# Optimization experiments

Measured on AMD Instinct MI355X. Metric: run time of the kernel, lower is better.

## Reference

```python
import jax, jax.numpy as jnp
import numpy as np

B, S, DM, H = 4, 1024, 1024, 16
DK = DM // H  # 64, must equal embeddim=64

def _linear(x, W, b):
    # torch nn.Linear: y = x @ W.T + b, W is [out, in]
    return jnp.matmul(x, W.T) + b

def setup_inputs() -> dict:
    key = jax.random.key(0)
    ks = jax.random.split(key, 40)
    inp = {}
    inp["query"] = jax.random.normal(ks[0], (B, S, DM), jnp.float32)
    inp["key"] = jax.random.normal(ks[1], (B, S, DM), jnp.float32)
    inp["value"] = jax.random.normal(ks[2], (B, S, DM), jnp.float32)
    inp["mask"] = jnp.ones((B, S, S), jnp.int32)
    def mk(i, dout, din):
        W = jax.random.normal(ks[i], (dout, din), jnp.float32) / np.sqrt(din).astype(np.float32)
        b = jax.random.normal(ks[i + 20], (dout,), jnp.float32) * 0.01
        return W, b
    # the 4 d_model x d_model projection linears (q, k, v, out)
    inp["Wq"], inp["bq"] = mk(3, DM, DM)
    inp["Wk"], inp["bk"] = mk(4, DM, DM)
    inp["Wv"], inp["bv"] = mk(5, DM, DM)
    inp["Wo"], inp["bo"] = mk(6, DM, DM)
    # the 64x64 refinement linears
    inp["Wkl"], inp["bkl"] = mk(7, DK, DK)   # key_linear
    inp["Wql"], inp["bql"] = mk(8, DK, DK)   # query_linear
    inp["Wq2"], inp["bq2"] = mk(9, DK, DK)   # query2_linear
    inp["Wvl"], inp["bvl"] = mk(10, DK, DK)  # value_linear
    inp["Wel"], inp["bel"] = mk(11, DK, DK)  # embed_linear
    return inp

def reference(query, key, value, mask,
              Wq, bq, Wk, bk, Wv, bv, Wo, bo,
              Wkl, bkl, Wql, bql, Wq2, bq2, Wvl, bvl, Wel, bel):
    b, s, dm = query.shape
    # project and split heads: [b, h, s, d_k]
    def split(x):
        return x.reshape(b, s, H, DK).transpose(0, 2, 1, 3)
    q = split(_linear(query, Wq, bq))
    k = split(_linear(key, Wk, bk))
    v = split(_linear(value, Wv, bv))
    # per-head 64x64 refinements with relu
    key_refine = jax.nn.relu(_linear(k, Wkl, bkl))
    q1 = jax.nn.relu(_linear(q, Wql, bql))
    q1 = jax.nn.relu(_linear(q1, Wel, bel))
    q2 = jax.nn.relu(_linear(q, Wq2, bq2))
    v_refine = jax.nn.relu(_linear(v, Wvl, bvl))
    # two attention-like matmuls (no 1/sqrt(d_k) scaling in original)
    qv = jnp.einsum("bhqd,bhkd->bhqk", q2, v_refine)
    kq = jnp.einsum("bhqd,bhkd->bhqk", q1, key_refine)
    m = mask[:, None, :, :]  # mask.unsqueeze(1)
    kq = jnp.where(m == 0, jnp.float32(-1e9), kq)
    attn = jax.nn.softmax(kq, axis=-1)
    # elementwise combine, then matmul against raw projected key (not value!)
    out = jnp.einsum("bhqk,bhkd->bhqd", attn * qv, k)
    out = out.transpose(0, 2, 1, 3).reshape(b, s, dm)
    return _linear(out, Wo, bo)
```

## Files before the change

kernel.cpp:

```cpp
#include <hip/hip_runtime.h>
#include <hip/hip_bf16.h>

#define B_  4
#define S_  1024
#define DM_ 1024
#define H_  16
#define DK_ 64
#define LOG2E 1.4426950408889634f

typedef unsigned short u16;
typedef __attribute__((ext_vector_type(8))) short bf16x8;
typedef __attribute__((ext_vector_type(4))) float f32x4;

__device__ __forceinline__ float bf2f(u16 u) {
    union { unsigned int i; float f; } c;
    c.i = ((unsigned int)u) << 16;
    return c.f;
}
__device__ __forceinline__ u16 f2bf(float f) {
    union { float f; unsigned int i; } c;
    c.f = f;
    unsigned int x = c.i;
    unsigned int lsb = (x >> 16) & 1u;
    x += 0x7fffu + lsb;
    return (u16)(x >> 16);
}
__device__ __forceinline__ u16 f2bf_fast(float f) {
    __hip_bfloat16 h = __float2bfloat16(f);
    return *reinterpret_cast<u16*>(&h);
}

__device__ __forceinline__ void async_ld16(const u16* g, u16* l) {
    __builtin_amdgcn_global_load_lds(
        (const __attribute__((address_space(1))) unsigned int*)(const void*)g,
        (__attribute__((address_space(3))) unsigned int*)(void*)l, 16, 0, 0);
}

__global__ void detect_kernel(const u16* __restrict__ q, int* __restrict__ flag) {
    int lane = threadIdx.x & 63;
    int cnt = 0;
#pragma unroll
    for (int i = 0; i < 4; ++i) {
        u16 u = q[2 * (lane * 4 + i)];
        int e = (u >> 7) & 0xFF;
        cnt += (e >= 100 && e <= 140) ? 1 : 0;
    }
#pragma unroll
    for (int off = 1; off < 64; off <<= 1) cnt += __shfl_xor(cnt, off, 64);
    if (lane == 0) *flag = (cnt < 128) ? 1 : 0;
}

#define NSEG 12
struct CvtArgs {
    const void* src[NSEG];
    void*       dst[NSEG];
    unsigned    off[NSEG + 1];
};

__global__ __launch_bounds__(256) void prep_kernel(
    CvtArgs a, unsigned total, const int* __restrict__ flag,
    const int* __restrict__ mask, int* __restrict__ tflags)
{
    const int tid = threadIdx.x;
    if (blockIdx.x < 512) {
        const int bx = blockIdx.x;
        const int kt = bx & 15, b = (bx >> 4) & 3, z = bx >> 6;
        int ok = 1;
#pragma unroll
        for (int i = tid; i < 128 * 16; i += 256) {
            int row = z * 128 + (i >> 4), seg = i & 15;
            int4 m = *(const int4*)&mask[((size_t)b * S_ + row) * S_ + kt * 64 + seg * 4];
            ok &= (m.x != 0) & (m.y != 0) & (m.z != 0) & (m.w != 0);
        }
        if (!ok) atomicOr(&tflags[b * 16 + kt], 1);
        return;
    }
    if (!*flag) return;
    unsigned v = (blockIdx.x - 512) * 256 + tid;
    if (v >= total) return;
    int s = 0;
    while (s < NSEG - 1 && v >= a.off[s + 1]) ++s;
    unsigned local = v - a.off[s];
    u16* dp = (u16*)a.dst[s] + (size_t)local * 8;
    const float* sp = (const float*)a.src[s] + (size_t)local * 8;
    float4 x = *(const float4*)sp, y = *(const float4*)(sp + 4);
    u16 t[8] = {f2bf(x.x), f2bf(x.y), f2bf(x.z), f2bf(x.w),
                f2bf(y.x), f2bf(y.y), f2bf(y.z), f2bf(y.w)};
    *(uint4*)dp = *(uint4*)t;
}

__global__ __launch_bounds__(256) void transpose_kernel(
    const u16* __restrict__ kp, u16* __restrict__ kpt)
{
    __shared__ u16 T[64][65];
    const int s0 = blockIdx.x * 64, h = blockIdx.y, b = blockIdx.z;
    const int tid = threadIdx.x;
    const size_t base = (size_t)b * S_ * DM_ + (size_t)h * DK_;
    for (int c = tid; c < 512; c += 256) {
        int row = c >> 3, cc = (c & 7) * 8;
        union { uint4 v; u16 u[8]; } x;
        x.v = *(const uint4*)&kp[base + (size_t)(s0 + row) * DM_ + cc];
#pragma unroll
        for (int j = 0; j < 8; ++j) T[row][cc + j] = x.u[j];
    }
    __syncthreads();
    const size_t baseT = (size_t)(b * H_ + h) * DK_ * S_;
    for (int c = tid; c < 512; c += 256) {
        int d = c >> 3, ss = (c & 7) * 8;
        u16 t[8];
#pragma unroll
        for (int j = 0; j < 8; ++j) t[j] = T[ss + j][d];
        *(uint4*)&kpt[baseT + (size_t)d * S_ + s0 + ss] = *(uint4*)t;
    }
}

struct GemmBatch {
    const u16* A0[4]; const u16* A1[4];
    const u16* W0[4]; const u16* W1[4];
    const u16* W20[4]; const u16* W21[4];
    const void* bias[4];
    const void* bias2[4];
    void* C[4];
    float oscale[4];
    int chain[4];
};

template<int ACT, int BIAS_DYN, int OUT_DYN>
__global__ __launch_bounds__(256, 3) void gemm_async_kernel(
    GemmBatch gb, int M, int N, int K, const int* __restrict__ flag)
{
    __shared__ __align__(16) u16 As[128][64];
    __shared__ __align__(16) u16 Ws[128][64];

    const int g = blockIdx.z;
    const int f = *flag;
    const u16* __restrict__ A = f ? gb.A1[g] : gb.A0[g];
    const u16* __restrict__ W = f ? gb.W1[g] : gb.W0[g];
    const void* biasp = gb.bias[g];
    void* Cp = gb.C[g];

    const int m0   = blockIdx.y * 128;
    const int n0   = blockIdx.x * 128;
    const int tid  = threadIdx.x;
    const int w    = tid >> 6;
    const int lane = tid & 63;
    const int l16  = lane & 15;
    const int quad = lane >> 4;
    const int wr   = (w >> 1) * 64;
    const int wc   = (w & 1) * 64;

    const int srow = lane >> 3;
    const int sgrp = (lane & 7) ^ srow;

    f32x4 acc[4][4];
#pragma unroll
    for (int rt = 0; rt < 4; ++rt)
#pragma unroll
        for (int ct = 0; ct < 4; ++ct) acc[rt][ct] = (f32x4){0.f, 0.f, 0.f, 0.f};

    for (int k0 = 0; k0 < K; k0 += 64) {
#pragma unroll
        for (int s = 0; s < 4; ++s) {
            int seg = w * 4 + s;
            async_ld16(&A[(size_t)(m0 + seg * 8 + srow) * K + k0 + sgrp * 8],
                       &As[seg * 8][0]);
            async_ld16(&W[(size_t)(n0 + seg * 8 + srow) * K + k0 + sgrp * 8],
                       &Ws[seg * 8][0]);
        }
        __syncthreads();
#pragma unroll
        for (int kk = 0; kk < 2; ++kk) {
            const int p = (kk * 4 + quad) ^ (l16 & 7);
            bf16x8 av[4], bv[4];
#pragma unroll
            for (int rt = 0; rt < 4; ++rt)
                av[rt] = *(const bf16x8*)&As[wr + rt * 16 + l16][p * 8];
#pragma unroll
            for (int ct = 0; ct < 4; ++ct)
                bv[ct] = *(const bf16x8*)&Ws[wc + ct * 16 + l16][p * 8];
#pragma unroll
            for (int rt = 0; rt < 4; ++rt)
#pragma unroll
                for (int ct = 0; ct < 4; ++ct)
                    acc[rt][ct] = __builtin_amdgcn_mfma_f32_16x16x32_bf16(
                        av[rt], bv[ct], acc[rt][ct], 0, 0, 0);
        }
        __syncthreads();
    }

#pragma unroll
    for (int ct = 0; ct < 4; ++ct) {
        int col = n0 + wc + ct * 16 + l16;
        float bv = (BIAS_DYN && f) ? ((const float*)biasp)[col]
                                   : bf2f(((const u16*)biasp)[col]);
#pragma unroll
        for (int rt = 0; rt < 4; ++rt)
#pragma unroll
            for (int r = 0; r < 4; ++r) {
                int row = m0 + wr + rt * 16 + quad * 4 + r;
                float v = acc[rt][ct][r] + bv;
                if (ACT) v = v > 0.f ? v : 0.f;
                size_t idx = (size_t)row * N + col;
                if (OUT_DYN && f) ((float*)Cp)[idx] = v;
                else              ((u16*)Cp)[idx]   = f2bf(v);
            }
    }
}

template<int ACT, int BIAS_DYN, int OUT_DYN>
__global__ __launch_bounds__(256, 2) void gemm_small_kernel(
    GemmBatch gb, int M, int N, int K, const int* __restrict__ flag)
{
    __shared__ __align__(16) u16 As[128][72];
    __shared__ __align__(16) u16 Ws[64][72];

    const int g = blockIdx.z;
    const int f = *flag;
    const u16* __restrict__ A = f ? gb.A1[g] : gb.A0[g];
    const u16* __restrict__ W = f ? gb.W1[g] : gb.W0[g];
    const void* biasp = gb.bias[g];
    void* Cp = gb.C[g];
    const float osc = gb.oscale[g];
    const int chain = gb.chain[g];

    const int m0   = blockIdx.y * 128;
    const int n0   = blockIdx.x * 64;
    const int tid  = threadIdx.x;
    const int w    = tid >> 6;
    const int lane = tid & 63;
    const int l16  = lane & 15;
    const int quad = lane >> 4;

    f32x4 acc[2][4];
#pragma unroll
    for (int rt = 0; rt < 2; ++rt)
#pragma unroll
        for (int ct = 0; ct < 4; ++ct) acc[rt][ct] = (f32x4){0.f, 0.f, 0.f, 0.f};

    for (int k0 = 0; k0 < K; k0 += 64) {
#pragma unroll
        for (int c = tid; c < 1024; c += 256) {
            int row = c >> 3, cc = (c & 7) * 8;
            *(uint4*)&As[row][cc] = *(const uint4*)&A[(size_t)(m0 + row) * K + k0 + cc];
        }
#pragma unroll
        for (int c = tid; c < 512; c += 256) {
            int row = c >> 3, cc = (c & 7) * 8;
            *(uint4*)&Ws[row][cc] = *(const uint4*)&W[(size_t)(n0 + row) * K + k0 + cc];
        }
        __syncthreads();
#pragma unroll
        for (int kk = 0; kk < 2; ++kk) {
            bf16x8 a[2], b[4];
#pragma unroll
            for (int rt = 0; rt < 2; ++rt)
                a[rt] = *(const bf16x8*)&As[w * 32 + rt * 16 + l16][kk * 32 + quad * 8];
#pragma unroll
            for (int ct = 0; ct < 4; ++ct)
                b[ct] = *(const bf16x8*)&Ws[ct * 16 + l16][kk * 32 + quad * 8];
#pragma unroll
            for (int rt = 0; rt < 2; ++rt)
#pragma unroll
                for (int ct = 0; ct < 4; ++ct)
                    acc[rt][ct] = __builtin_amdgcn_mfma_f32_16x16x32_bf16(
                        a[rt], b[ct], acc[rt][ct], 0, 0, 0);
        }
        __syncthreads();
    }

    if (!chain) {
#pragma unroll
        for (int ct = 0; ct < 4; ++ct) {
            int col = n0 + ct * 16 + l16;
            float bv = (BIAS_DYN && f) ? ((const float*)biasp)[col]
                                       : bf2f(((const u16*)biasp)[col]);
#pragma unroll
            for (int rt = 0; rt < 2; ++rt)
#pragma unroll
                for (int r = 0; r < 4; ++r) {
                    int row = m0 + w * 32 + rt * 16 + quad * 4 + r;
                    float v = acc[rt][ct][r] + bv;
                    if (ACT) v = v > 0.f ? v : 0.f;
                    v *= osc;
                    size_t idx = (size_t)row * N + col;
                    if (OUT_DYN && f) ((float*)Cp)[idx] = v;
                    else              ((u16*)Cp)[idx]   = f2bf(v);
                }
        }
    } else {
        const u16* __restrict__ W2 = f ? gb.W21[g] : gb.W20[g];
#pragma unroll
        for (int c = tid; c < 512; c += 256) {
            int row = c >> 3, cc = (c & 7) * 8;
            *(uint4*)&Ws[row][cc] = *(const uint4*)&W2[(size_t)row * 64 + cc];
        }
#pragma unroll
        for (int ct = 0; ct < 4; ++ct) {
            int col = ct * 16 + l16;
            float bv = (BIAS_DYN && f) ? ((const float*)biasp)[col]
                                       : bf2f(((const u16*)biasp)[col]);
#pragma unroll
            for (int rt = 0; rt < 2; ++rt)
#pragma unroll
                for (int r = 0; r < 4; ++r) {
                    float v = acc[rt][ct][r] + bv;
                    v = v > 0.f ? v : 0.f;
                    As[w * 32 + rt * 16 + quad * 4 + r][col] = f2bf(v);
                }
        }
        __syncthreads();

        f32x4 acc2[2][4];
#pragma unroll
        for (int rt = 0; rt < 2; ++rt)
#pragma unroll
            for (int ct = 0; ct < 4; ++ct) acc2[rt][ct] = (f32x4){0.f, 0.f, 0.f, 0.f};
#pragma unroll
        for (int kk = 0; kk < 2; ++kk) {
            bf16x8 a[2], b[4];
#pragma unroll
            for (int rt = 0; rt < 2; ++rt)
                a[rt] = *(const bf16x8*)&As[w * 32 + rt * 16 + l16][kk * 32 + quad * 8];
#pragma unroll
            for (int ct = 0; ct < 4; ++ct)
                b[ct] = *(const bf16x8*)&Ws[ct * 16 + l16][kk * 32 + quad * 8];
#pragma unroll
            for (int rt = 0; rt < 2; ++rt)
#pragma unroll
                for (int ct = 0; ct < 4; ++ct)
                    acc2[rt][ct] = __builtin_amdgcn_mfma_f32_16x16x32_bf16(
                        a[rt], b[ct], acc2[rt][ct], 0, 0, 0);
        }
#pragma unroll
        for (int ct = 0; ct < 4; ++ct) {
            int col = ct * 16 + l16;
            float bv2 = (BIAS_DYN && f) ? ((const float*)gb.bias2[g])[col]
                                        : bf2f(((const u16*)gb.bias2[g])[col]);
#pragma unroll
            for (int rt = 0; rt < 2; ++rt)
#pragma unroll
                for (int r = 0; r < 4; ++r) {
                    int row = m0 + w * 32 + rt * 16 + quad * 4 + r;
                    float v = acc2[rt][ct][r] + bv2;
                    v = v > 0.f ? v : 0.f;
                    v *= osc;
                    ((u16*)Cp)[(size_t)row * N + col] = f2bf(v);
                }
        }
    }
}

__global__ __launch_bounds__(256, 2) void attn_kernel(
    const u16* __restrict__ q1, const u16* __restrict__ q2,
    const u16* __restrict__ kr, const u16* __restrict__ vr,
    const u16* __restrict__ kpt, const int* __restrict__ mask,
    const int* __restrict__ tflags, u16* __restrict__ om)
{
    __shared__ __align__(16) u16 krs[64][72];
    __shared__ __align__(16) u16 vrs[64][72];
    __shared__ __align__(16) u16 kts[64][72];
    __shared__ __align__(16) u16 pts[4][32][72];

    const int qt   = blockIdx.x;
    const int h    = blockIdx.y;
    const int b    = blockIdx.z;
    const int q0   = qt * 128;
    const int tid  = threadIdx.x;
    const int w    = tid >> 6;
    const int lane = tid & 63;
    const int l16  = lane & 15;
    const int quad = lane >> 4;

    const size_t base  = (size_t)b * S_ * DM_ + (size_t)h * DK_;
    const size_t baseT = (size_t)(b * H_ + h) * DK_ * S_;

    bf16x8 a1[2][2], a2[2][2];
#pragma unroll
    for (int rt = 0; rt < 2; ++rt) {
        const int qrow = q0 + w * 32 + rt * 16 + l16;
#pragma unroll
        for (int kk = 0; kk < 2; ++kk) {
            a1[rt][kk] = *(const bf16x8*)&q1[base + (size_t)qrow * DM_ + kk * 32 + quad * 8];
            a2[rt][kk] = *(const bf16x8*)&q2[base + (size_t)qrow * DM_ + kk * 32 + quad * 8];
        }
    }

    float m_run[2][4], l_run[2][4];
    f32x4 oacc[2][4];
#pragma unroll
    for (int rt = 0; rt < 2; ++rt)
#pragma unroll
        for (int r = 0; r < 4; ++r) { m_run[rt][r] = -1e30f; l_run[rt][r] = 0.f; }
#pragma unroll
    for (int rt = 0; rt < 2; ++rt)
#pragma unroll
        for (int ct = 0; ct < 4; ++ct) oacc[rt][ct] = (f32x4){0.f, 0.f, 0.f, 0.f};

    for (int kt = 0; kt < S_ / 64; ++kt) {
        const int k0 = kt * 64;
        __syncthreads();
        for (int c = tid; c < 512; c += 256) {
            int row = c >> 3, cc = (c & 7) * 8;
            *(uint4*)&krs[row][cc] = *(const uint4*)&kr[base + (size_t)(k0 + row) * DM_ + cc];
            *(uint4*)&vrs[row][cc] = *(const uint4*)&vr[base + (size_t)(k0 + row) * DM_ + cc];
            *(uint4*)&kts[row][cc] = *(const uint4*)&kpt[baseT + (size_t)row * S_ + k0 + cc];
        }
        __syncthreads();

        const int tf = tflags[b * 16 + kt];

        f32x4 s1[2][4], s2[2][4];
#pragma unroll
        for (int rt = 0; rt < 2; ++rt)
#pragma unroll
            for (int ct = 0; ct < 4; ++ct) {
                s1[rt][ct] = (f32x4){0.f, 0.f, 0.f, 0.f};
                s2[rt][ct] = (f32x4){0.f, 0.f, 0.f, 0.f};
            }
#pragma unroll
        for (int kk = 0; kk < 2; ++kk) {
            bf16x8 b1[4], b2[4];
#pragma unroll
            for (int ct = 0; ct < 4; ++ct) {
                b1[ct] = *(const bf16x8*)&krs[ct * 16 + l16][kk * 32 + quad * 8];
                b2[ct] = *(const bf16x8*)&vrs[ct * 16 + l16][kk * 32 + quad * 8];
            }
#pragma unroll
            for (int rt = 0; rt < 2; ++rt)
#pragma unroll
                for (int ct = 0; ct < 4; ++ct) {
                    s1[rt][ct] = __builtin_amdgcn_mfma_f32_16x16x32_bf16(
                        a1[rt][kk], b1[ct], s1[rt][ct], 0, 0, 0);
                    s2[rt][ct] = __builtin_amdgcn_mfma_f32_16x16x32_bf16(
                        a2[rt][kk], b2[ct], s2[rt][ct], 0, 0, 0);
                }
        }

        if (tf) {
#pragma unroll
            for (int rt = 0; rt < 2; ++rt)
#pragma unroll
                for (int ct = 0; ct < 4; ++ct)
#pragma unroll
                    for (int r = 0; r < 4; ++r) {
                        int qrow = q0 + w * 32 + rt * 16 + quad * 4 + r;
                        int kc   = k0 + ct * 16 + l16;
                        if (mask[((size_t)b * S_ + qrow) * S_ + kc] == 0)
                            s1[rt][ct][r] = -1e9f;
                    }
        }

        float tmax[2][4];
#pragma unroll
        for (int rt = 0; rt < 2; ++rt)
#pragma unroll
            for (int r = 0; r < 4; ++r) tmax[rt][r] = -1e30f;
#pragma unroll
        for (int rt = 0; rt < 2; ++rt)
#pragma unroll
            for (int ct = 0; ct < 4; ++ct)
#pragma unroll
                for (int r = 0; r < 4; ++r)
                    tmax[rt][r] = fmaxf(tmax[rt][r], s1[rt][ct][r]);
#pragma unroll
        for (int off = 1; off < 16; off <<= 1)
#pragma unroll
            for (int rt = 0; rt < 2; ++rt)
#pragma unroll
                for (int r = 0; r < 4; ++r)
                    tmax[rt][r] = fmaxf(tmax[rt][r], __shfl_xor(tmax[rt][r], off, 64));

        float alpha[2][4], newm[2][4];
#pragma unroll
        for (int rt = 0; rt < 2; ++rt)
#pragma unroll
            for (int r = 0; r < 4; ++r) {
                newm[rt][r]  = fmaxf(m_run[rt][r], tmax[rt][r]);
                alpha[rt][r] = exp2f(m_run[rt][r] - newm[rt][r]);
                m_run[rt][r] = newm[rt][r];
            }

        float psum[2][4] = {};
#pragma unroll
        for (int rt = 0; rt < 2; ++rt)
#pragma unroll
            for (int ct = 0; ct < 4; ++ct)
#pragma unroll
                for (int r = 0; r < 4; ++r) {
                    float p = exp2f(s1[rt][ct][r] - newm[rt][r]);
                    psum[rt][r] += p;
                    pts[w][rt * 16 + quad * 4 + r][ct * 16 + l16] =
                        f2bf_fast(p * s2[rt][ct][r]);
                }
#pragma unroll
        for (int off = 1; off < 16; off <<= 1)
#pragma unroll
            for (int rt = 0; rt < 2; ++rt)
#pragma unroll
                for (int r = 0; r < 4; ++r)
                    psum[rt][r] += __shfl_xor(psum[rt][r], off, 64);
#pragma unroll
        for (int rt = 0; rt < 2; ++rt)
#pragma unroll
            for (int r = 0; r < 4; ++r)
                l_run[rt][r] = l_run[rt][r] * alpha[rt][r] + psum[rt][r];
#pragma unroll
        for (int rt = 0; rt < 2; ++rt)
#pragma unroll
            for (int ct = 0; ct < 4; ++ct)
#pragma unroll
                for (int r = 0; r < 4; ++r) oacc[rt][ct][r] *= alpha[rt][r];

        {
            bf16x8 bb[2][4];
#pragma unroll
            for (int kk = 0; kk < 2; ++kk)
#pragma unroll
                for (int ct = 0; ct < 4; ++ct)
                    bb[kk][ct] = *(const bf16x8*)&kts[ct * 16 + l16][kk * 32 + quad * 8];
#pragma unroll
            for (int rt = 0; rt < 2; ++rt)
#pragma unroll
                for (int kk = 0; kk < 2; ++kk) {
                    bf16x8 a = *(const bf16x8*)&pts[w][rt * 16 + l16][kk * 32 + quad * 8];
#pragma unroll
                    for (int ct = 0; ct < 4; ++ct)
                        oacc[rt][ct] = __builtin_amdgcn_mfma_f32_16x16x32_bf16(
                            a, bb[kk][ct], oacc[rt][ct], 0, 0, 0);
                }
        }
    }

#pragma unroll
    for (int rt = 0; rt < 2; ++rt)
#pragma unroll
        for (int ct = 0; ct < 4; ++ct)
#pragma unroll
            for (int r = 0; r < 4; ++r) {
                int row = q0 + w * 32 + rt * 16 + quad * 4 + r;
                int col = ct * 16 + l16;
                float v = oacc[rt][ct][r] / l_run[rt][r];
                om[base + (size_t)row * DM_ + col] = f2bf_fast(v);
            }
}

extern "C" void kernel_launch(void* const* d_in, const int* in_sizes, int n_in,
                              void* d_out, int out_size, void* d_ws, size_t ws_size,
                              hipStream_t stream)
{
    const void* query = d_in[0];
    const void* key   = d_in[1];
    const void* value = d_in[2];
    const int*  mask  = (const int*)d_in[3];
    const void* Wq  = d_in[4];  const void* bq  = d_in[5];
    const void* Wk  = d_in[6];  const void* bk  = d_in[7];
    const void* Wv  = d_in[8];  const void* bv  = d_in[9];
    const void* Wo  = d_in[10]; const void* bo  = d_in[11];
    const void* Wkl = d_in[12]; const void* bkl = d_in[13];
    const void* Wql = d_in[14]; const void* bql = d_in[15];
    const void* Wq2 = d_in[16]; const void* bq2 = d_in[17];
    const void* Wvl = d_in[18]; const void* bvl = d_in[19];
    const void* Wel = d_in[20]; const void* bel = d_in[21];

    int* flag   = (int*)d_ws;
    int* tflags = (int*)d_ws + 4;
    u16* ws     = (u16*)((char*)d_ws + 512);
    const size_t BUF = (size_t)(B_ * S_) * DM_;
    u16* Qp  = ws + 0 * BUF;
    u16* Kp  = ws + 1 * BUF;
    u16* Vp  = ws + 2 * BUF;
    u16* krb = ws + 3 * BUF;
    u16* q1b = ws + 4 * BUF;
    u16* q2r = ws + 5 * BUF;
    u16* vrb = ws + 6 * BUF;
    u16* Om  = ws + 7 * BUF;
    u16* Qc  = ws + 8 * BUF;
    u16* Kc  = ws + 9 * BUF;
    u16* Vc  = ws + 10 * BUF;
    u16* Wbig = ws + 11 * BUF;
    u16* Wqc = Wbig + 0 * (size_t)(DM_ * DM_);
    u16* Wkc = Wbig + 1 * (size_t)(DM_ * DM_);
    u16* Wvc = Wbig + 2 * (size_t)(DM_ * DM_);
    u16* Woc = Wbig + 3 * (size_t)(DM_ * DM_);
    u16* Wsm = Wbig + 4 * (size_t)(DM_ * DM_);
    u16* Wklc = Wsm + 0 * (DK_ * DK_);
    u16* Wqlc = Wsm + 1 * (DK_ * DK_);
    u16* Welc = Wsm + 2 * (DK_ * DK_);
    u16* Wq2c = Wsm + 3 * (DK_ * DK_);
    u16* Wvlc = Wsm + 4 * (DK_ * DK_);
    u16* KpT = Vp;

    const int M = B_ * S_;
    dim3 blk(256);

    detect_kernel<<<1, 64, 0, stream>>>((const u16*)query, flag);

    hipMemsetAsync(tflags, 0, 64 * sizeof(int), stream);
    CvtArgs ca;
    const unsigned VIN = (unsigned)(BUF / 8);
    const unsigned VWB = (unsigned)(DM_ * DM_ / 8);
    const unsigned VWS = (unsigned)(DK_ * DK_ / 8);
    const void* srcs[NSEG] = {query, key, value, Wq, Wk, Wv, Wo, Wkl, Wql, Wel, Wq2, Wvl};
    void* dsts[NSEG] = {Qc, Kc, Vc, Wqc, Wkc, Wvc, Woc, Wklc, Wqlc, Welc, Wq2c, Wvlc};
    unsigned vcn[NSEG] = {VIN, VIN, VIN, VWB, VWB, VWB, VWB, VWS, VWS, VWS, VWS, VWS};
    unsigned off = 0;
    for (int i = 0; i < NSEG; ++i) { ca.src[i] = srcs[i]; ca.dst[i] = dsts[i]; ca.off[i] = off; off += vcn[i]; }
    ca.off[NSEG] = off;
    prep_kernel<<<dim3(512 + (off + 255) / 256), blk, 0, stream>>>(ca, off, flag, mask, tflags);

    GemmBatch gqkv = {};
    gqkv.A0[0] = (const u16*)query; gqkv.A1[0] = Qc;
    gqkv.A0[1] = (const u16*)key;   gqkv.A1[1] = Kc;
    gqkv.A0[2] = (const u16*)value; gqkv.A1[2] = Vc;
    gqkv.W0[0] = (const u16*)Wq; gqkv.W1[0] = Wqc;
    gqkv.W0[1] = (const u16*)Wk; gqkv.W1[1] = Wkc;
    gqkv.W0[2] = (const u16*)Wv; gqkv.W1[2] = Wvc;
    gqkv.bias[0] = bq; gqkv.bias[1] = bk; gqkv.bias[2] = bv;
    gqkv.C[0] = Qp; gqkv.C[1] = Kp; gqkv.C[2] = Vp;
    dim3 gBig(DM_ / 128, M / 128, 3);
    gemm_async_kernel<0,1,0><<<gBig, blk, 0, stream>>>(gqkv, M, DM_, DM_, flag);

    GemmBatch gref = {};
    gref.A0[0] = gref.A1[0] = Kp; gref.W0[0] = (const u16*)Wkl; gref.W1[0] = Wklc;
    gref.A0[1] = gref.A1[1] = Qp; gref.W0[1] = (const u16*)Wql; gref.W1[1] = Wqlc;
    gref.A0[2] = gref.A1[2] = Qp; gref.W0[2] = (const u16*)Wq2; gref.W1[2] = Wq2c;
    gref.A0[3] = gref.A1[3] = Vp; gref.W0[3] = (const u16*)Wvl; gref.W1[3] = Wvlc;
    gref.bias[0] = bkl; gref.bias[1] = bql; gref.bias[2] = bq2; gref.bias[3] = bvl;
    gref.C[0] = krb; gref.C[1] = q1b; gref.C[2] = q2r; gref.C[3] = vrb;
    gref.oscale[0] = 1.0f; gref.oscale[1] = LOG2E; gref.oscale[2] = 1.0f; gref.oscale[3] = 1.0f;
    gref.chain[0] = 0; gref.chain[1] = 1; gref.chain[2] = 0; gref.chain[3] = 0;
    gref.W20[1] = (const u16*)Wel; gref.W21[1] = Welc; gref.bias2[1] = bel;
    dim3 gSm(1, (M * H_) / 128, 4);
    gemm_small_kernel<1,1,0><<<gSm, blk, 0, stream>>>(gref, M * H_, DK_, DK_, flag);

    dim3 gT(S_ / 64, H_, B_);
    transpose_kernel<<<gT, blk, 0, stream>>>(Kp, KpT);

    dim3 gA(S_ / 128, H_, B_);
    attn_kernel<<<gA, blk, 0, stream>>>(q1b, q2r, krb, vrb, KpT, mask, tflags, Om);

    GemmBatch go = {};
    go.A0[0] = go.A1[0] = Om; go.W0[0] = (const u16*)Wo; go.W1[0] = Woc;
    go.bias[0] = bo; go.C[0] = (u16*)d_out;
    dim3 gO(DM_ / 128, M / 128, 1);
    gemm_async_kernel<0,1,1><<<gO, blk, 0, stream>>>(go, M, DM_, DM_, flag);
}
```

Measured before the change: 316.7 us.

## Fuse per-head refinement linears into QKV projection GEMM epilogue

The QKV projection kernel now runs the 64x64 refinement linears (key, value, query1 chain, query2) in its epilogue. The projected tile is staged in swizzled shared memory and reused as the MFMA A operand, so the Q and V projections are never written to global memory and the separate small-GEMM launch is removed. The LOG2E prescale on q1 is dropped and the softmax switches from exp2f to __expf. The epilogue adds register and shared-memory pressure, which may lower occupancy of the large GEMM, and the q-head blocks do serial extra work.

```diff
diff --git a/kernel.cpp b/kernel.cpp
--- a/kernel.cpp
+++ b/kernel.cpp
@@ -6,7 +6,6 @@
 #define DM_ 1024
 #define H_  16
 #define DK_ 64
-#define LOG2E 1.4426950408889634f
 
 typedef unsigned short u16;
 typedef __attribute__((ext_vector_type(8))) short bf16x8;
@@ -114,30 +113,29 @@
     }
 }
 
-struct GemmBatch {
-    const u16* A0[4]; const u16* A1[4];
-    const u16* W0[4]; const u16* W1[4];
-    const u16* W20[4]; const u16* W21[4];
-    const void* bias[4];
-    const void* bias2[4];
-    void* C[4];
-    float oscale[4];
-    int chain[4];
+struct QKVArgs {
+    const u16* A0[3]; const u16* A1[3];
+    const u16* W0[3]; const u16* W1[3];
+    const void* bias[3];
+    const u16* R10[3]; const u16* R11[3];
+    const void* rb1[3];
+    const u16* R20; const u16* R21; const void* rb2;
+    const u16* R30; const u16* R31; const void* rb3;
+    u16 *Kp, *q1b, *q2r, *krb, *vrb;
 };
 
-template<int ACT, int BIAS_DYN, int OUT_DYN>
-__global__ __launch_bounds__(256, 3) void gemm_async_kernel(
-    GemmBatch gb, int M, int N, int K, const int* __restrict__ flag)
+__global__ __launch_bounds__(256, 3) void qkv_fused_kernel(
+    QKVArgs a, const int* __restrict__ flag)
 {
-    __shared__ __align__(16) u16 As[128][64];
-    __shared__ __align__(16) u16 Ws[128][64];
-
-    const int g = blockIdx.z;
+    __shared__ __align__(16) u16 smem[16384];
+    u16 (*As)[64] = (u16(*)[64])smem;
+    u16 (*Ws)[64] = (u16(*)[64])(smem + 8192);
+
+    const int z = blockIdx.z;
     const int f = *flag;
-    const u16* __restrict__ A = f ? gb.A1[g] : gb.A0[g];
-    const u16* __restrict__ W = f ? gb.W1[g] : gb.W0[g];
-    const void* biasp = gb.bias[g];
-    void* Cp = gb.C[g];
+    const u16* __restrict__ A = f ? a.A1[z] : a.A0[z];
+    const u16* __restrict__ W = f ? a.W1[z] : a.W0[z];
+    const void* biasp = a.bias[z];
 
     const int m0   = blockIdx.y * 128;
     const int n0   = blockIdx.x * 128;
@@ -158,13 +156,13 @@
 #pragma unroll
         for (int ct = 0; ct < 4; ++ct) acc[rt][ct] = (f32x4){0.f, 0.f, 0.f, 0.f};
 
-    for (int k0 = 0; k0 < K; k0 += 64) {
+    for (int k0 = 0; k0 < DM_; k0 += 64) {
 #pragma unroll
         for (int s = 0; s < 4; ++s) {
             int seg = w * 4 + s;
-            async_ld16(&A[(size_t)(m0 + seg * 8 + srow) * K + k0 + sgrp * 8],
+            async_ld16(&A[(size_t)(m0 + seg * 8 + srow) * DM_ + k0 + sgrp * 8],
                        &As[seg * 8][0]);
-            async_ld16(&W[(size_t)(n0 + seg * 8 + srow) * K + k0 + sgrp * 8],
+            async_ld16(&W[(size_t)(n0 + seg * 8 + srow) * DM_ + k0 + sgrp * 8],
                        &Ws[seg * 8][0]);
         }
         __syncthreads();
@@ -188,165 +186,248 @@
         __syncthreads();
     }
 
+    const int hcol = n0 + wc;
+    u16 (*Es)[64] = (u16(*)[64])(smem + w * 4096);
+
 #pragma unroll
     for (int ct = 0; ct < 4; ++ct) {
-        int col = n0 + wc + ct * 16 + l16;
-        float bv = (BIAS_DYN && f) ? ((const float*)biasp)[col]
-                                   : bf2f(((const u16*)biasp)[col]);
+        int col = hcol + ct * 16 + l16;
+        float bv = f ? ((const float*)biasp)[col] : bf2f(((const u16*)biasp)[col]);
 #pragma unroll
         for (int rt = 0; rt < 4; ++rt)
 #pragma unroll
             for (int r = 0; r < 4; ++r) {
-                int row = m0 + wr + rt * 16 + quad * 4 + r;
-                float v = acc[rt][ct][r] + bv;
-                if (ACT) v = v > 0.f ? v : 0.f;
-                size_t idx = (size_t)row * N + col;
-                if (OUT_DYN && f) ((float*)Cp)[idx] = v;
-                else              ((u16*)Cp)[idx]   = f2bf(v);
-            }
-    }
-}
-
-template<int ACT, int BIAS_DYN, int OUT_DYN>
-__global__ __launch_bounds__(256, 2) void gemm_small_kernel(
-    GemmBatch gb, int M, int N, int K, const int* __restrict__ flag)
+                int ml = rt * 16 + quad * 4 + r;
+                int cl = ct * 16 + l16;
+                u16 bb = f2bf(acc[rt][ct][r] + bv);
+                if (z == 1) a.Kp[(size_t)(m0 + wr + ml) * DM_ + col] = bb;
+                Es[ml][((((cl >> 3) ^ (ml & 7)) << 3) | (cl & 7))] = bb;
+            }
+    }
+
+    bf16x8 af[4][2];
+#pragma unroll
+    for (int rt = 0; rt < 4; ++rt)
+#pragma unroll
+        for (int kk = 0; kk < 2; ++kk)
+            af[rt][kk] = *(const bf16x8*)
+                &Es[rt * 16 + l16][(((kk * 4 + quad) ^ (l16 & 7)) << 3)];
+
+    const u16* R1 = f ? a.R11[z] : a.R10[z];
+    bf16x8 wb[2][4];
+#pragma unroll
+    for (int kk = 0; kk < 2; ++kk)
+#pragma unroll
+        for (int ct = 0; ct < 4; ++ct)
+            wb[kk][ct] = *(const bf16x8*)
+                &R1[(size_t)(ct * 16 + l16) * 64 + kk * 32 + quad * 8];
+
+    f32x4 r1[4][4];
+#pragma unroll
+    for (int rt = 0; rt < 4; ++rt)
+#pragma unroll
+        for (int ct = 0; ct < 4; ++ct) r1[rt][ct] = (f32x4){0.f, 0.f, 0.f, 0.f};
+#pragma unroll
+    for (int kk = 0; kk < 2; ++kk)
+#pragma unroll
+        for (int rt = 0; rt < 4; ++rt)
+#pragma unroll
+            for (int ct = 0; ct < 4; ++ct)
+                r1[rt][ct] = __builtin_amdgcn_mfma_f32_16x16x32_bf16(
+                    af[rt][kk], wb[kk][ct], r1[rt][ct], 0, 0, 0);
+
+    if (z != 0) {
+        const void* rb = a.rb1[z];
+        u16* out = (z == 1) ? a.krb : a.vrb;
+#pragma unroll
+        for (int ct = 0; ct < 4; ++ct) {
+            int cl = ct * 16 + l16;
+            float bv = f ? ((const float*)rb)[cl] : bf2f(((const u16*)rb)[cl]);
+#pragma unroll
+            for (int rt = 0; rt < 4; ++rt)
+#pragma unroll
+                for (int r = 0; r < 4; ++r) {
+                    float v = r1[rt][ct][r] + bv;
+                    v = v > 0.f ? v : 0.f;
+                    out[(size_t)(m0 + wr + rt * 16 + quad * 4 + r) * DM_ + hcol + cl]
+                        = f2bf(v);
+                }
+        }
+    } else {
+        {
+            const void* rb = a.rb1[0];
+#pragma unroll
+            for (int ct = 0; ct < 4; ++ct) {
+                int cl = ct * 16 + l16;
+                float bv = f ? ((const float*)rb)[cl] : bf2f(((const u16*)rb)[cl]);
+#pragma unroll
+                for (int rt = 0; rt < 4; ++rt)
+#pragma unroll
+                    for (int r = 0; r < 4; ++r) {
+                        float v = r1[rt][ct][r] + bv;
+                        v = v > 0.f ? v : 0.f;
+                        int ml = rt * 16 + quad * 4 + r;
+                        Es[ml][((((cl >> 3) ^ (ml & 7)) << 3) | (cl & 7))] = f2bf(v);
+                    }
+            }
+        }
+        {
+            const u16* R3 = f ? a.R31 : a.R30;
+#pragma unroll
+            for (int kk = 0; kk < 2; ++kk)
+#pragma unroll
+                for (int ct = 0; ct < 4; ++ct)
+                    wb[kk][ct] = *(const bf16x8*)
+                        &R3[(size_t)(ct * 16 + l16) * 64 + kk * 32 + quad * 8];
+            f32x4 r3[4][4];
+#pragma unroll
+            for (int rt = 0; rt < 4; ++rt)
+#pragma unroll
+                for (int ct = 0; ct < 4; ++ct) r3[rt][ct] = (f32x4){0.f, 0.f, 0.f, 0.f};
+#pragma unroll
+            for (int kk = 0; kk < 2; ++kk)
+#pragma unroll
+                for (int rt = 0; rt < 4; ++rt)
+#pragma unroll
+                    for (int ct = 0; ct < 4; ++ct)
+                        r3[rt][ct] = __builtin_amdgcn_mfma_f32_16x16x32_bf16(
+                            af[rt][kk], wb[kk][ct], r3[rt][ct], 0, 0, 0);
+            const void* rb = a.rb3;
+#pragma unroll
+            for (int ct = 0; ct < 4; ++ct) {
+                int cl = ct * 16 + l16;
+                float bv = f ? ((const float*)rb)[cl] : bf2f(((const u16*)rb)[cl]);
+#pragma unroll
+                for (int rt = 0; rt < 4; ++rt)
+#pragma unroll
+                    for (int r = 0; r < 4; ++r) {
+                        float v = r3[rt][ct][r] + bv;
+                        v = v > 0.f ? v : 0.f;
+                        a.q2r[(size_t)(m0 + wr + rt * 16 + quad * 4 + r) * DM_
+                              + hcol + cl] = f2bf(v);
+                    }
+            }
+        }
+        {
+#pragma unroll
+            for (int rt = 0; rt < 4; ++rt)
+#pragma unroll
+                for (int kk = 0; kk < 2; ++kk)
+                    af[rt][kk] = *(const bf16x8*)
+                        &Es[rt * 16 + l16][(((kk * 4 + quad) ^ (l16 & 7)) << 3)];
+            const u16* R2 = f ? a.R21 : a.R20;
+#pragma unroll
+            for (int kk = 0; kk < 2; ++kk)
+#pragma unroll
+                for (int ct = 0; ct < 4; ++ct)
+                    wb[kk][ct] = *(const bf16x8*)
+                        &R2[(size_t)(ct * 16 + l16) * 64 + kk * 32 + quad * 8];
+            f32x4 r2[4][4];
+#pragma unroll
+            for (int rt = 0; rt < 4; ++rt)
+#pragma unroll
+                for (int ct = 0; ct < 4; ++ct) r2[rt][ct] = (f32x4){0.f, 0.f, 0.f, 0.f};
+#pragma unroll
+            for (int kk = 0; kk < 2; ++kk)
+#pragma unroll
+                for (int rt = 0; rt < 4; ++rt)
+#pragma unroll
+                    for (int ct = 0; ct < 4; ++ct)
+                        r2[rt][ct] = __builtin_amdgcn_mfma_f32_16x16x32_bf16(
+                            af[rt][kk], wb[kk][ct], r2[rt][ct], 0, 0, 0);
+            const void* rb = a.rb2;
+#pragma unroll
+            for (int ct = 0; ct < 4; ++ct) {
+                int cl = ct * 16 + l16;
+                float bv = f ? ((const float*)rb)[cl] : bf2f(((const u16*)rb)[cl]);
+#pragma unroll
+                for (int rt = 0; rt < 4; ++rt)
+#pragma unroll
+                    for (int r = 0; r < 4; ++r) {
+                        float v = r2[rt][ct][r] + bv;
+                        v = v > 0.f ? v : 0.f;
+                        a.q1b[(size_t)(m0 + wr + rt * 16 + quad * 4 + r) * DM_
+                              + hcol + cl] = f2bf(v);
+                    }
+            }
+        }
+    }
+}
+
+__global__ __launch_bounds__(256, 3) void gemm_async_kernel(
+    const u16* __restrict__ Ain, const u16* __restrict__ W0,
+    const u16* __restrict__ W1, const void* __restrict__ biasp,
+    void* __restrict__ Cp, const int* __restrict__ flag)
 {
-    __shared__ __align__(16) u16 As[128][72];
-    __shared__ __align__(16) u16 Ws[64][72];
-
-    const int g = blockIdx.z;
+    __shared__ __align__(16) u16 As[128][64];
+    __shared__ __align__(16) u16 Ws[128][64];
+
     const int f = *flag;
-    const u16* __restrict__ A = f ? gb.A1[g] : gb.A0[g];
-    const u16* __restrict__ W = f ? gb.W1[g] : gb.W0[g];
-    const void* biasp = gb.bias[g];
-    void* Cp = gb.C[g];
-    const float osc = gb.oscale[g];
-    const int chain = gb.chain[g];
+    const u16* __restrict__ W = f ? W1 : W0;
 
     const int m0   = blockIdx.y * 128;
-    const int n0   = blockIdx.x * 64;
+    const int n0   = blockIdx.x * 128;
     const int tid  = threadIdx.x;
     const int w    = tid >> 6;
     const int lane = tid & 63;
     const int l16  = lane & 15;
     const int quad = lane >> 4;
-
-    f32x4 acc[2][4];
-#pragma unroll
-    for (int rt = 0; rt < 2; ++rt)
+    const int wr   = (w >> 1) * 64;
+    const int wc   = (w & 1) * 64;
+
+    const int srow = lane >> 3;
+    const int sgrp = (lane & 7) ^ srow;
+
+    f32x4 acc[4][4];
+#pragma unroll
+    for (int rt = 0; rt < 4; ++rt)
 #pragma unroll
         for (int ct = 0; ct < 4; ++ct) acc[rt][ct] = (f32x4){0.f, 0.f, 0.f, 0.f};
 
-    for (int k0 = 0; k0 < K; k0 += 64) {
-#pragma unroll
-        for (int c = tid; c < 1024; c += 256) {
-            int row = c >> 3, cc = (c & 7) * 8;
-            *(uint4*)&As[row][cc] = *(const uint4*)&A[(size_t)(m0 + row) * K + k0 + cc];
-        }
-#pragma unroll
-        for (int c = tid; c < 512; c += 256) {
-            int row = c >> 3, cc = (c & 7) * 8;
-            *(uint4*)&Ws[row][cc] = *(const uint4*)&W[(size_t)(n0 + row) * K + k0 + cc];
+    for (int k0 = 0; k0 < DM_; k0 += 64) {
+#pragma unroll
+        for (int s = 0; s < 4; ++s) {
+            int seg = w * 4 + s;
+            async_ld16(&Ain[(size_t)(m0 + seg * 8 + srow) * DM_ + k0 + sgrp * 8],
+                       &As[seg * 8][0]);
+            async_ld16(&W[(size_t)(n0 + seg * 8 + srow) * DM_ + k0 + sgrp * 8],
+                       &Ws[seg * 8][0]);
         }
         __syncthreads();
 #pragma unroll
         for (int kk = 0; kk < 2; ++kk) {
-            bf16x8 a[2], b[4];
-#pragma unroll
-            for (int rt = 0; rt < 2; ++rt)
-                a[rt] = *(const bf16x8*)&As[w * 32 + rt * 16 + l16][kk * 32 + quad * 8];
+            const int p = (kk * 4 + quad) ^ (l16 & 7);
+            bf16x8 av[4], bv[4];
+#pragma unroll
+            for (int rt = 0; rt < 4; ++rt)
+                av[rt] = *(const bf16x8*)&As[wr + rt * 16 + l16][p * 8];
 #pragma unroll
             for (int ct = 0; ct < 4; ++ct)
-                b[ct] = *(const bf16x8*)&Ws[ct * 16 + l16][kk * 32 + quad * 8];
-#pragma unroll
-            for (int rt = 0; rt < 2; ++rt)
+                bv[ct] = *(const bf16x8*)&Ws[wc + ct * 16 + l16][p * 8];
+#pragma unroll
+            for (int rt = 0; rt < 4; ++rt)
 #pragma unroll
                 for (int ct = 0; ct < 4; ++ct)
                     acc[rt][ct] = __builtin_amdgcn_mfma_f32_16x16x32_bf16(
-                        a[rt], b[ct], acc[rt][ct], 0, 0, 0);
+                        av[rt], bv[ct], acc[rt][ct], 0, 0, 0);
         }
         __syncthreads();
     }
 
-    if (!chain) {
-#pragma unroll
-        for (int ct = 0; ct < 4; ++ct) {
-            int col = n0 + ct * 16 + l16;
-            float bv = (BIAS_DYN && f) ? ((const float*)biasp)[col]
-                                       : bf2f(((const u16*)biasp)[col]);
-#pragma unroll
-            for (int rt = 0; rt < 2; ++rt)
-#pragma unroll
-                for (int r = 0; r < 4; ++r) {
-                    int row = m0 + w * 32 + rt * 16 + quad * 4 + r;
-                    float v = acc[rt][ct][r] + bv;
-                    if (ACT) v = v > 0.f ? v : 0.f;
-                    v *= osc;
-                    size_t idx = (size_t)row * N + col;
-                    if (OUT_DYN && f) ((float*)Cp)[idx] = v;
-                    else              ((u16*)Cp)[idx]   = f2bf(v);
-                }
-        }
-    } else {
-        const u16* __restrict__ W2 = f ? gb.W21[g] : gb.W20[g];
-#pragma unroll
-        for (int c = tid; c < 512; c += 256) {
-            int row = c >> 3, cc = (c & 7) * 8;
-            *(uint4*)&Ws[row][cc] = *(const uint4*)&W2[(size_t)row * 64 + cc];
-        }
-#pragma unroll
-        for (int ct = 0; ct < 4; ++ct) {
-            int col = ct * 16 + l16;
-            float bv = (BIAS_DYN && f) ? ((const float*)biasp)[col]
-                                       : bf2f(((const u16*)biasp)[col]);
-#pragma unroll
-            for (int rt = 0; rt < 2; ++rt)
-#pragma unroll
-                for (int r = 0; r < 4; ++r) {
-                    float v = acc[rt][ct][r] + bv;
-                    v = v > 0.f ? v : 0.f;
-                    As[w * 32 + rt * 16 + quad * 4 + r][col] = f2bf(v);
-                }
-        }
-        __syncthreads();
-
-        f32x4 acc2[2][4];
-#pragma unroll
-        for (int rt = 0; rt < 2; ++rt)
-#pragma unroll
-            for (int ct = 0; ct < 4; ++ct) acc2[rt][ct] = (f32x4){0.f, 0.f, 0.f, 0.f};
-#pragma unroll
-        for (int kk = 0; kk < 2; ++kk) {
-            bf16x8 a[2], b[4];
-#pragma unroll
-            for (int rt = 0; rt < 2; ++rt)
-                a[rt] = *(const bf16x8*)&As[w * 32 + rt * 16 + l16][kk * 32 + quad * 8];
-#pragma unroll
-            for (int ct = 0; ct < 4; ++ct)
-                b[ct] = *(const bf16x8*)&Ws[ct * 16 + l16][kk * 32 + quad * 8];
-#pragma unroll
-            for (int rt = 0; rt < 2; ++rt)
-#pragma unroll
-                for (int ct = 0; ct < 4; ++ct)
-                    acc2[rt][ct] = __builtin_amdgcn_mfma_f32_16x16x32_bf16(
-                        a[rt], b[ct], acc2[rt][ct], 0, 0, 0);
-        }
-#pragma unroll
-        for (int ct = 0; ct < 4; ++ct) {
-            int col = ct * 16 + l16;
-            float bv2 = (BIAS_DYN && f) ? ((const float*)gb.bias2[g])[col]
-                                        : bf2f(((const u16*)gb.bias2[g])[col]);
-#pragma unroll
-            for (int rt = 0; rt < 2; ++rt)
-#pragma unroll
-                for (int r = 0; r < 4; ++r) {
-                    int row = m0 + w * 32 + rt * 16 + quad * 4 + r;
-                    float v = acc2[rt][ct][r] + bv2;
-                    v = v > 0.f ? v : 0.f;
-                    v *= osc;
-                    ((u16*)Cp)[(size_t)row * N + col] = f2bf(v);
-                }
-        }
+#pragma unroll
+    for (int ct = 0; ct < 4; ++ct) {
+        int col = n0 + wc + ct * 16 + l16;
+        float bv = f ? ((const float*)biasp)[col] : bf2f(((const u16*)biasp)[col]);
+#pragma unroll
+        for (int rt = 0; rt < 4; ++rt)
+#pragma unroll
+            for (int r = 0; r < 4; ++r) {
+                int row = m0 + wr + rt * 16 + quad * 4 + r;
+                float v = acc[rt][ct][r] + bv;
+                size_t idx = (size_t)row * DM_ + col;
+                if (f) ((float*)Cp)[idx] = v;
+                else   ((u16*)Cp)[idx]   = f2bf(v);
+            }
     }
 }
 
@@ -476,7 +557,7 @@
 #pragma unroll
             for (int r = 0; r < 4; ++r) {
                 newm[rt][r]  = fmaxf(m_run[rt][r], tmax[rt][r]);
-                alpha[rt][r] = exp2f(m_run[rt][r] - newm[rt][r]);
+                alpha[rt][r] = __expf(m_run[rt][r] - newm[rt][r]);
                 m_run[rt][r] = newm[rt][r];
             }
 
@@ -487,7 +568,7 @@
             for (int ct = 0; ct < 4; ++ct)
 #pragma unroll
                 for (int r = 0; r < 4; ++r) {
-                    float p = exp2f(s1[rt][ct][r] - newm[rt][r]);
+                    float p = __expf(s1[rt][ct][r] - newm[rt][r]);
                     psum[rt][r] += p;
                     pts[w][rt * 16 + quad * 4 + r][ct * 16 + l16] =
                         f2bf_fast(p * s2[rt][ct][r]);
@@ -566,18 +647,17 @@
     int* tflags = (int*)d_ws + 4;
     u16* ws     = (u16*)((char*)d_ws + 512);
     const size_t BUF = (size_t)(B_ * S_) * DM_;
-    u16* Qp  = ws + 0 * BUF;
-    u16* Kp  = ws + 1 * BUF;
-    u16* Vp  = ws + 2 * BUF;
-    u16* krb = ws + 3 * BUF;
-    u16* q1b = ws + 4 * BUF;
-    u16* q2r = ws + 5 * BUF;
-    u16* vrb = ws + 6 * BUF;
-    u16* Om  = ws + 7 * BUF;
-    u16* Qc  = ws + 8 * BUF;
-    u16* Kc  = ws + 9 * BUF;
-    u16* Vc  = ws + 10 * BUF;
-    u16* Wbig = ws + 11 * BUF;
+    u16* Kp  = ws + 0 * BUF;
+    u16* krb = ws + 1 * BUF;
+    u16* q1b = ws + 2 * BUF;
+    u16* q2r = ws + 3 * BUF;
+    u16* vrb = ws + 4 * BUF;
+    u16* Om  = ws + 5 * BUF;
+    u16* KpT = ws + 6 * BUF;
+    u16* Qc  = ws + 7 * BUF;
+    u16* Kc  = ws + 8 * BUF;
+    u16* Vc  = ws + 9 * BUF;
+    u16* Wbig = ws + 10 * BUF;
     u16* Wqc = Wbig + 0 * (size_t)(DM_ * DM_);
     u16* Wkc = Wbig + 1 * (size_t)(DM_ * DM_);
     u16* Wvc = Wbig + 2 * (size_t)(DM_ * DM_);
@@ -588,7 +668,6 @@
     u16* Welc = Wsm + 2 * (DK_ * DK_);
     u16* Wq2c = Wsm + 3 * (DK_ * DK_);
     u16* Wvlc = Wsm + 4 * (DK_ * DK_);
-    u16* KpT = Vp;
 
     const int M = B_ * S_;
     dim3 blk(256);
@@ -608,30 +687,22 @@
     ca.off[NSEG] = off;
     prep_kernel<<<dim3(512 + (off + 255) / 256), blk, 0, stream>>>(ca, off, flag, mask, tflags);
 
-    GemmBatch gqkv = {};
-    gqkv.A0[0] = (const u16*)query; gqkv.A1[0] = Qc;
-    gqkv.A0[1] = (const u16*)key;   gqkv.A1[1] = Kc;
-    gqkv.A0[2] = (const u16*)value; gqkv.A1[2] = Vc;
-    gqkv.W0[0] = (const u16*)Wq; gqkv.W1[0] = Wqc;
-    gqkv.W0[1] = (const u16*)Wk; gqkv.W1[1] = Wkc;
-    gqkv.W0[2] = (const u16*)Wv; gqkv.W1[2] = Wvc;
-    gqkv.bias[0] = bq; gqkv.bias[1] = bk; gqkv.bias[2] = bv;
-    gqkv.C[0] = Qp; gqkv.C[1] = Kp; gqkv.C[2] = Vp;
+    QKVArgs qa = {};
+    qa.A0[0] = (const u16*)query; qa.A1[0] = Qc;
+    qa.A0[1] = (const u16*)key;   qa.A1[1] = Kc;
+    qa.A0[2] = (const u16*)value; qa.A1[2] = Vc;
+    qa.W0[0] = (const u16*)Wq; qa.W1[0] = Wqc;
+    qa.W0[1] = (const u16*)Wk; qa.W1[1] = Wkc;
+    qa.W0[2] = (const u16*)Wv; qa.W1[2] = Wvc;
+    qa.bias[0] = bq; qa.bias[1] = bk; qa.bias[2] = bv;
+    qa.R10[0] = (const u16*)Wql; qa.R11[0] = Wqlc; qa.rb1[0] = bql;
+    qa.R10[1] = (const u16*)Wkl; qa.R11[1] = Wklc; qa.rb1[1] = bkl;
+    qa.R10[2] = (const u16*)Wvl; qa.R11[2] = Wvlc; qa.rb1[2] = bvl;
+    qa.R20 = (const u16*)Wel; qa.R21 = Welc; qa.rb2 = bel;
+    qa.R30 = (const u16*)Wq2; qa.R31 = Wq2c; qa.rb3 = bq2;
+    qa.Kp = Kp; qa.q1b = q1b; qa.q2r = q2r; qa.krb = krb; qa.vrb = vrb;
     dim3 gBig(DM_ / 128, M / 128, 3);
-    gemm_async_kernel<0,1,0><<<gBig, blk, 0, stream>>>(gqkv, M, DM_, DM_, flag);
-
-    GemmBatch gref = {};
-    gref.A0[0] = gref.A1[0] = Kp; gref.W0[0] = (const u16*)Wkl; gref.W1[0] = Wklc;
-    gref.A0[1] = gref.A1[1] = Qp; gref.W0[1] = (const u16*)Wql; gref.W1[1] = Wqlc;
-    gref.A0[2] = gref.A1[2] = Qp; gref.W0[2] = (const u16*)Wq2; gref.W1[2] = Wq2c;
-    gref.A0[3] = gref.A1[3] = Vp; gref.W0[3] = (const u16*)Wvl; gref.W1[3] = Wvlc;
-    gref.bias[0] = bkl; gref.bias[1] = bql; gref.bias[2] = bq2; gref.bias[3] = bvl;
-    gref.C[0] = krb; gref.C[1] = q1b; gref.C[2] = q2r; gref.C[3] = vrb;
-    gref.oscale[0] = 1.0f; gref.oscale[1] = LOG2E; gref.oscale[2] = 1.0f; gref.oscale[3] = 1.0f;
-    gref.chain[0] = 0; gref.chain[1] = 1; gref.chain[2] = 0; gref.chain[3] = 0;
-    gref.W20[1] = (const u16*)Wel; gref.W21[1] = Welc; gref.bias2[1] = bel;
-    dim3 gSm(1, (M * H_) / 128, 4);
-    gemm_small_kernel<1,1,0><<<gSm, blk, 0, stream>>>(gref, M * H_, DK_, DK_, flag);
+    qkv_fused_kernel<<<gBig, blk, 0, stream>>>(qa, flag);
 
     dim3 gT(S_ / 64, H_, B_);
     transpose_kernel<<<gT, blk, 0, stream>>>(Kp, KpT);
@@ -639,9 +710,6 @@
     dim3 gA(S_ / 128, H_, B_);
     attn_kernel<<<gA, blk, 0, stream>>>(q1b, q2r, krb, vrb, KpT, mask, tflags, Om);
 
-    GemmBatch go = {};
-    go.A0[0] = go.A1[0] = Om; go.W0[0] = (const u16*)Wo; go.W1[0] = Woc;
-    go.bias[0] = bo; go.C[0] = (u16*)d_out;
-    dim3 gO(DM_ / 128, M / 128, 1);
-    gemm_async_kernel<0,1,1><<<gO, blk, 0, stream>>>(go, M, DM_, DM_, flag);
-}
+    dim3 gO(DM_ / 128, M / 128);
+    gemm_async_kernel<<<gO, blk, 0, stream>>>(Om, (const u16*)Wo, Woc, bo, d_out, flag);
+}
```

Result: no change. 315.5 us (-0.4%).
